# Kernel tuning notes

Measured on AMD Instinct MI355X. Metric: run time of the kernel, lower is better.

Reference implementation:

```python
import jax, jax.numpy as jnp
import numpy as np

B = 4; E_PER = 100_000; E = B * E_PER
N_NODES = 50_000; N_REL = 500; D = 64; D_LG = 256
K_PER_VI = 20; S_VI = E // K_PER_VI          # 20000 sorted vi segments
S_VJ_PER = 5_000; S_VJ = B * S_VJ_PER        # 20000 unsorted vj segments
N_MEM = 131_072
INTERACT = ((0, 3), (0, 2, 3), (0, 4), (0, 2, 4), (1, 3), (1, 2, 3), (1, 4), (1, 2, 4))


def _build_edges():
    rng = np.random.default_rng(0)
    idx_vi = np.repeat(np.arange(S_VI), K_PER_VI)          # sorted segment ids
    gpb = S_VI // B
    eg = idx_vi // gpb                                     # sorted by eg_idx too
    vi = rng.integers(0, N_NODES, S_VI)[idx_vi]
    idx_vj = np.empty(E, dtype=np.int64)
    for b in range(B):
        loc = np.concatenate([np.arange(S_VJ_PER), rng.integers(0, S_VJ_PER, E_PER - S_VJ_PER)])
        rng.shuffle(loc)
        idx_vj[b * E_PER:(b + 1) * E_PER] = b * S_VJ_PER + loc  # every group non-empty
    vj = rng.integers(0, N_NODES, S_VJ)[idx_vj]            # consistent (eg, vj) per group
    rel = rng.integers(0, N_REL, E)
    e2vi = rng.integers(0, N_MEM, E)
    e2vj = rng.integers(0, N_MEM, E)
    return np.stack([eg, vi, vj, rel, idx_vi, idx_vj, e2vi, e2vj], axis=1).astype(np.int32)


def setup_inputs() -> dict:
    key = jax.random.key(0)
    ks = jax.random.split(key, 10)
    return {
        "node_attention": jax.random.uniform(ks[0], (B, N_NODES), jnp.float32),
        "scanned_edges": jnp.asarray(_build_edges()),
        "edges_y": jax.random.uniform(ks[1], (E,), jnp.float32),
        "hidden_uncon": jax.random.normal(ks[2], (1, N_NODES, D_LG), jnp.float32),
        "hidden_con": jax.random.normal(ks[3], (N_MEM, D), jnp.float32),
        "Wc": jax.random.normal(ks[4], (D, D), jnp.float32) / np.sqrt(D).astype(np.float32),
        "bc": jnp.zeros((D,), jnp.float32),
        "Wu": jax.random.normal(ks[5], (D_LG, D), jnp.float32) / np.sqrt(D_LG).astype(np.float32),
        "bu": jnp.zeros((D,), jnp.float32),
        "rel_table": jax.random.normal(ks[6], (N_REL, D), jnp.float32) * 0.05,
        "ws": jax.random.normal(ks[7], (len(INTERACT), D), jnp.float32) / np.sqrt(float(len(INTERACT))).astype(np.float32) if False else jax.random.normal(ks[7], (len(INTERACT), D), jnp.float32) * (1.0 / np.sqrt(len(INTERACT)).astype(np.float32)),
        "fb": jnp.zeros((D,), jnp.float32),
        "out_w": jax.random.normal(ks[8], (D,), jnp.float32),
        "out_b": jnp.zeros((D,), jnp.float32),
        "n_vi_segments": S_VI,
        "n_vj_segments": S_VJ,
    }


def reference(node_attention, scanned_edges, edges_y, hidden_uncon, hidden_con,
              Wc, bc, Wu, bu, rel_table, ws, fb, out_w, out_b,
              n_vi_segments, n_vj_segments):
    eg, vi, vj, rel = (scanned_edges[:, i] for i in range(4))
    idx_vi, idx_vj, e2vi, e2vj = (scanned_edges[:, i] for i in range(4, 8))
    # projections (proj_con / proj_uncon, tanh Dense)
    hc = jnp.tanh(hidden_con @ Wc + bc)          # [N_MEM, D]
    hu = jnp.tanh(hidden_uncon @ Wu + bu)[0]     # [n_nodes, D]; batch_size==1 path of Node2Edge
    # Node2Edge gathers
    feats = (hc[e2vi], hu[vi], rel_table[rel], hc[e2vj], hu[vj])  # each [E, D]
    # F layer: weighted sum of elementwise interaction products
    out = fb
    for k, idxs in enumerate(INTERACT):
        x = feats[idxs[0]]
        for i in idxs[1:]:
            x = x * feats[i]
        out = out + x * ws[k]
    out = jax.nn.relu(out) * out_w + out_b
    logits = jnp.sum(out, axis=1)                # [E]
    # NeighborSoftmax at 'vi' (sorted segment softmax)
    m = jax.ops.segment_max(logits, idx_vi, num_segments=n_vi_segments)
    ex = jnp.exp(logits - m[idx_vi])
    den = jax.ops.segment_sum(ex, idx_vi, num_segments=n_vi_segments)
    transition = ex / den[idx_vi]
    # attention flow: gather source attention, weight, aggregate at vj
    trans_att = transition * node_attention[eg, vi] * edges_y
    aggr = jax.ops.segment_sum(trans_att, idx_vj, num_segments=n_vj_segments)
    b_g = jax.ops.segment_max(eg, idx_vj, num_segments=n_vj_segments)
    vj_g = jax.ops.segment_max(vj, idx_vj, num_segments=n_vj_segments)
    new_node_attention = jnp.zeros_like(node_attention).at[b_g, vj_g].add(aggr)
    return new_node_attention
```

## Files before the change

kernel.cpp:

```cpp
#include <hip/hip_runtime.h>
#include <hip/hip_bf16.h>
#include <type_traits>

#define D 64
#define KPER 20

typedef __attribute__((ext_vector_type(8))) short short8;
typedef __attribute__((ext_vector_type(4))) float floatx4;

__device__ __forceinline__ unsigned short f2bfu(float x) {
    __hip_bfloat16 h = __float2bfloat16(x);
    return *reinterpret_cast<unsigned short*>(&h);
}
__device__ __forceinline__ float bfu2f(unsigned short u) {
    return __uint_as_float(((unsigned)u) << 16);
}

__device__ __forceinline__ float fast_tanh(float x) {
    float xc = fminf(fmaxf(x, -15.f), 15.f);
    float e = __expf(2.f * xc);
    return 1.f - 2.f * __builtin_amdgcn_rcpf(1.f + e);
}

template<int CTRL>
__device__ __forceinline__ float dpp_add(float x) {
    int t = __builtin_amdgcn_update_dpp(0, __float_as_int(x), CTRL, 0xf, 0xf, true);
    return x + __int_as_float(t);
}
template<int CTRL>
__device__ __forceinline__ float dpp_max(float x) {
    int xi = __float_as_int(x);
    int t = __builtin_amdgcn_update_dpp(xi, xi, CTRL, 0xf, 0xf, false);
    return fmaxf(x, __int_as_float(t));
}
__device__ __forceinline__ float wave_sum_b(float x) {
    x = dpp_add<0x111>(x); x = dpp_add<0x112>(x);
    x = dpp_add<0x114>(x); x = dpp_add<0x118>(x);
    x = dpp_add<0x142>(x); x = dpp_add<0x143>(x);
    return __int_as_float(__builtin_amdgcn_readlane(__float_as_int(x), 63));
}
__device__ __forceinline__ float wave_max_b(float x) {
    x = dpp_max<0x111>(x); x = dpp_max<0x112>(x);
    x = dpp_max<0x114>(x); x = dpp_max<0x118>(x);
    x = dpp_max<0x142>(x); x = dpp_max<0x143>(x);
    return __int_as_float(__builtin_amdgcn_readlane(__float_as_int(x), 63));
}
__device__ __forceinline__ float row16_sum(float x) {
    x = dpp_add<0x111>(x); x = dpp_add<0x112>(x);
    x = dpp_add<0x114>(x); x = dpp_add<0x118>(x);
    return x;
}

__device__ __forceinline__ void proj64_pair(const float* __restrict__ h,
        const float* __restrict__ W, const float* __restrict__ b,
        unsigned short* __restrict__ out, int rt0) {
    constexpr int K = 64, KT = 2, CTN = 4;
    int lane = threadIdx.x & 63;
    int m = lane & 15, quad = lane >> 4;
    short8 bfr[CTN][KT];
    #pragma unroll
    for (int ct = 0; ct < CTN; ++ct)
        #pragma unroll
        for (int kt = 0; kt < KT; ++kt)
            #pragma unroll
            for (int j = 0; j < 8; ++j)
                bfr[ct][kt][j] = (short)f2bfu(W[(size_t)(kt * 32 + quad * 8 + j) * 64 + ct * 16 + m]);
    float bv[CTN];
    #pragma unroll
    for (int ct = 0; ct < CTN; ++ct) bv[ct] = b[ct * 16 + m];
    int rt1 = rt0 + 1;
    const float* hrow0 = h + (size_t)(rt0 * 16 + m) * K + quad * 8;
    const float* hrow1 = h + (size_t)(rt1 * 16 + m) * K + quad * 8;
    floatx4 a0[KT][2], a1[KT][2];
    #pragma unroll
    for (int kt = 0; kt < KT; ++kt) {
        a0[kt][0] = *(const floatx4*)(hrow0 + kt * 32);
        a0[kt][1] = *(const floatx4*)(hrow0 + kt * 32 + 4);
        a1[kt][0] = *(const floatx4*)(hrow1 + kt * 32);
        a1[kt][1] = *(const floatx4*)(hrow1 + kt * 32 + 4);
    }
    #pragma unroll
    for (int t = 0; t < 2; ++t) {
        floatx4 (*ar)[2] = t ? a1 : a0;
        int rt = t ? rt1 : rt0;
        floatx4 acc[CTN];
        #pragma unroll
        for (int ct = 0; ct < CTN; ++ct) acc[ct] = floatx4{0.f, 0.f, 0.f, 0.f};
        #pragma unroll
        for (int kt = 0; kt < KT; ++kt) {
            short8 af;
            #pragma unroll
            for (int j = 0; j < 4; ++j) {
                af[j]     = (short)f2bfu(ar[kt][0][j]);
                af[j + 4] = (short)f2bfu(ar[kt][1][j]);
            }
            #pragma unroll
            for (int ct = 0; ct < CTN; ++ct)
                acc[ct] = __builtin_amdgcn_mfma_f32_16x16x32_bf16(af, bfr[ct][kt], acc[ct], 0, 0, 0);
        }
        #pragma unroll
        for (int ct = 0; ct < CTN; ++ct) {
            int col = ct * 16 + m;
            #pragma unroll
            for (int reg = 0; reg < 4; ++reg) {
                int row = rt * 16 + quad * 4 + reg;
                out[(size_t)row * 64 + col] = f2bfu(fast_tanh(acc[ct][reg] + bv[ct]));
            }
        }
    }
}

__device__ __forceinline__ void proj256_body(const float* __restrict__ h,
        const float* __restrict__ W, const float* __restrict__ b,
        unsigned short* __restrict__ out, int ct0, int rt0, int rtstride, int ntiles) {
    constexpr int K = 256, KT = 8, CTN = 2;
    int lane = threadIdx.x & 63;
    int m = lane & 15, quad = lane >> 4;
    short8 bfr[CTN][KT];
    #pragma unroll
    for (int ct = 0; ct < CTN; ++ct)
        #pragma unroll
        for (int kt = 0; kt < KT; ++kt)
            #pragma unroll
            for (int j = 0; j < 8; ++j)
                bfr[ct][kt][j] = (short)f2bfu(W[(size_t)(kt * 32 + quad * 8 + j) * 64 + (ct0 + ct) * 16 + m]);
    float bv[CTN];
    #pragma unroll
    for (int ct = 0; ct < CTN; ++ct) bv[ct] = b[(ct0 + ct) * 16 + m];
    for (int rt = rt0; rt < ntiles; rt += rtstride) {
        floatx4 acc[CTN];
        #pragma unroll
        for (int ct = 0; ct < CTN; ++ct) acc[ct] = floatx4{0.f, 0.f, 0.f, 0.f};
        const float* hrow = h + (size_t)(rt * 16 + m) * K + quad * 8;
        #pragma unroll
        for (int kt = 0; kt < KT; ++kt) {
            floatx4 v0 = *(const floatx4*)(hrow + kt * 32);
            floatx4 v1 = *(const floatx4*)(hrow + kt * 32 + 4);
            short8 af;
            #pragma unroll
            for (int j = 0; j < 4; ++j) {
                af[j]     = (short)f2bfu(v0[j]);
                af[j + 4] = (short)f2bfu(v1[j]);
            }
            #pragma unroll
            for (int ct = 0; ct < CTN; ++ct)
                acc[ct] = __builtin_amdgcn_mfma_f32_16x16x32_bf16(af, bfr[ct][kt], acc[ct], 0, 0, 0);
        }
        #pragma unroll
        for (int ct = 0; ct < CTN; ++ct) {
            int col = (ct0 + ct) * 16 + m;
            #pragma unroll
            for (int reg = 0; reg < 4; ++reg) {
                int row = rt * 16 + quad * 4 + reg;
                out[(size_t)row * 64 + col] = f2bfu(fast_tanh(acc[ct][reg] + bv[ct]));
            }
        }
    }
}

#define RELB 16
#define ZB 8
__global__ __launch_bounds__(256) void proj_fused(
        const float* __restrict__ hcon, const float* __restrict__ Wc, const float* __restrict__ bc,
        const float* __restrict__ hun, const float* __restrict__ Wu, const float* __restrict__ bu,
        const float* __restrict__ relf, unsigned short* __restrict__ hc,
        unsigned short* __restrict__ hu, unsigned short* __restrict__ relb,
        float* __restrict__ outz, int nout,
        int t64, int t256, int g64, int g256, int nrel) {
    int bid = blockIdx.x;
    int w = threadIdx.x >> 6;
    if (bid < g64) {
        int wid = bid * 4 + w;
        proj64_pair(hcon, Wc, bc, hc, wid * 2);
    } else if (bid < g64 + g256) {
        int wid = (bid - g64) * 4 + w;
        int half = wid & 1;
        proj256_body(hun, Wu, bu, hu, half * 2, wid >> 1, (g256 * 4) >> 1, t256);
    } else if (bid < g64 + g256 + RELB) {
        int tid = (bid - g64 - g256) * 256 + threadIdx.x;
        for (int i = tid; i < nrel; i += RELB * 256) relb[i] = f2bfu(relf[i]);
    } else {
        int tid = (bid - g64 - g256 - RELB) * 256 + threadIdx.x;
        for (int i = tid; i < nout; i += ZB * 256) outz[i] = 0.0f;
    }
}

__device__ __forceinline__ void unp4(uint2 u, float f[4]) {
    f[0] = __uint_as_float(u.x << 16);
    f[1] = __uint_as_float(u.x & 0xffff0000u);
    f[2] = __uint_as_float(u.y << 16);
    f[3] = __uint_as_float(u.y & 0xffff0000u);
}

__global__ __launch_bounds__(256) void edge_kernel(
        const float* __restrict__ natt, const int* __restrict__ edges,
        const float* __restrict__ ey, const unsigned short* __restrict__ hc,
        const unsigned short* __restrict__ hu, const unsigned short* __restrict__ relt,
        const float* __restrict__ wsm, const float* __restrict__ fb,
        const float* __restrict__ outw, float* __restrict__ out, int N) {
    int lane = threadIdx.x & 63;
    int g = lane >> 4, sub = lane & 15;
    int l2 = lane >> 2;
    int s = blockIdx.x * 4 + (threadIdx.x >> 6);
    long base = (long)s * KPER;
    const int* eb = edges + base * 8;
    int eg = __builtin_amdgcn_readfirstlane(eb[0]);
    int vi = __builtin_amdgcn_readfirstlane(eb[1]);

    const int* ebg = eb + g * 8;
    int vjx[5], relx[5], evix[5], evjx[5];
    #pragma unroll
    for (int i = 0; i < 5; ++i) {
        vjx[i]  = ebg[i * 32 + 2];
        relx[i] = ebg[i * 32 + 3];
        evix[i] = ebg[i * 32 + 6];
        evjx[i] = ebg[i * 32 + 7];
    }
    uint2 G0[5], G2[5], G3[5], G4[5];
    #pragma unroll
    for (int i = 0; i < 5; ++i) {
        G0[i] = *(const uint2*)(hc   + (size_t)evix[i] * D + sub * 4);
        G2[i] = *(const uint2*)(relt + (size_t)relx[i] * D + sub * 4);
        G3[i] = *(const uint2*)(hc   + (size_t)evjx[i] * D + sub * 4);
        G4[i] = *(const uint2*)(hu   + (size_t)vjx[i]  * D + sub * 4);
    }
    uint2 F1u = *(const uint2*)(hu + (size_t)vi * D + sub * 4);
    float f1[4];
    unp4(F1u, f1);

    floatx4 wv[8];
    #pragma unroll
    for (int k = 0; k < 8; ++k) wv[k] = *(const floatx4*)(wsm + k * D + sub * 4);
    floatx4 fbv = *(const floatx4*)(fb + sub * 4);
    floatx4 owv = *(const floatx4*)(outw + sub * 4);
    float na = natt[(size_t)eg * N + vi];

    float myl = -INFINITY;
    #pragma unroll
    for (int i = 0; i < 5; ++i) {
        float F0[4], F2[4], F3[4], F4[4];
        unp4(G0[i], F0); unp4(G2[i], F2); unp4(G3[i], F3); unp4(G4[i], F4);
        float acc = 0.f;
        #pragma unroll
        for (int j = 0; j < 4; ++j) {
            float t1 = fmaf(F2[j], wv[1][j], wv[0][j]);
            float t2 = fmaf(F2[j], wv[5][j], wv[4][j]);
            float t3 = fmaf(F2[j], wv[3][j], wv[2][j]);
            float t4 = fmaf(F2[j], wv[7][j], wv[6][j]);
            float u = fmaf(F0[j], t1, f1[j] * t2);
            float v = fmaf(F0[j], t3, f1[j] * t4);
            float od = fmaf(F3[j], u, fmaf(F4[j], v, fbv[j]));
            acc = fmaf(fmaxf(od, 0.f), owv[j], acc);
        }
        float rs = row16_sum(acc);
        float tot = __shfl(rs, ((lane & 3) << 4) + 15);
        myl = (l2 == i) ? tot : myl;
    }
    float mx = wave_max_b(myl);
    float ex = __expf(myl - mx);
    float den = wave_sum_b(ex);
    if (lane < KPER) {
        int myvj = eb[lane * 8 + 2];
        float t = (ex / den) * na * ey[base + lane];
        atomicAdd(out + (size_t)eg * N + myvj, t);
    }
}

extern "C" void kernel_launch(void* const* d_in, const int* in_sizes, int n_in,
                              void* d_out, int out_size, void* d_ws, size_t ws_size,
                              hipStream_t stream) {
    const float* natt = (const float*)d_in[0];
    const int*   edges = (const int*)d_in[1];
    const float* ey   = (const float*)d_in[2];
    const float* hun  = (const float*)d_in[3];
    const float* hcon = (const float*)d_in[4];
    const float* Wc   = (const float*)d_in[5];
    const float* bc   = (const float*)d_in[6];
    const float* Wu   = (const float*)d_in[7];
    const float* bu   = (const float*)d_in[8];
    const float* relt = (const float*)d_in[9];
    const float* wsm  = (const float*)d_in[10];
    const float* fb   = (const float*)d_in[11];
    const float* outw = (const float*)d_in[12];
    float* out = (float*)d_out;

    int E    = in_sizes[2];
    int S    = E / KPER;
    int nmem = in_sizes[4] / D;
    int N    = in_sizes[3] / 256;
    int nrel = in_sizes[9];

    int t64  = nmem / 16;
    int t256 = N / 16;
    int g64  = t64 / 8;
    int g256 = 512;

    unsigned short* hc = (unsigned short*)d_ws;
    unsigned short* hu = hc + (size_t)nmem * D;
    unsigned short* rb = hu + (size_t)N * D;

    proj_fused<<<g64 + g256 + RELB + ZB, 256, 0, stream>>>(hcon, Wc, bc, hun, Wu, bu,
                                                           relt, hc, hu, rb,
                                                           out, out_size,
                                                           t64, t256, g64, g256, nrel);
    edge_kernel<<<S / 4, 256, 0, stream>>>(natt, edges, ey, hc, hu, rb,
                                           wsm, fb, outw, out, N);
}
```

Measured before the change: 203.6 us.

## Pre-pack bf16 MFMA weight fragments in a prep kernel and reorder projection blocks

Adds a small prep kernel that converts Wc and Wu to bf16 once, in MFMA fragment order, and also handles the relation-table conversion and output zeroing. The projection waves then load each B fragment with one vector load instead of eight strided scalar loads plus conversions. The 256-wide projection blocks are placed first and their count rises from 512 to 800. This adds one extra kernel launch and a dependency between launches in exchange for cheaper per-wave weight setup.

```diff
diff --git a/kernel.cpp b/kernel.cpp
--- a/kernel.cpp
+++ b/kernel.cpp
@@ -51,8 +51,32 @@
     return x;
 }
 
+__global__ __launch_bounds__(256) void prep(
+        const float* __restrict__ Wc, const float* __restrict__ Wu,
+        const float* __restrict__ relf,
+        unsigned short* __restrict__ Wcp, unsigned short* __restrict__ Wup,
+        unsigned short* __restrict__ relb, float* __restrict__ outz,
+        int nout, int nrel) {
+    int tid = blockIdx.x * 256 + threadIdx.x;
+    int nth = gridDim.x * 256;
+    for (int i = tid; i < 4 * 2 * 64 * 8; i += nth) {
+        int j = i & 7, lane = (i >> 3) & 63, f = i >> 9;
+        int ct = f >> 1, kt = f & 1;
+        int m = lane & 15, quad = lane >> 4;
+        Wcp[i] = f2bfu(Wc[(kt * 32 + quad * 8 + j) * 64 + ct * 16 + m]);
+    }
+    for (int i = tid; i < 4 * 8 * 64 * 8; i += nth) {
+        int j = i & 7, lane = (i >> 3) & 63, f = i >> 9;
+        int ct = f >> 3, kt = f & 7;
+        int m = lane & 15, quad = lane >> 4;
+        Wup[i] = f2bfu(Wu[(kt * 32 + quad * 8 + j) * 64 + ct * 16 + m]);
+    }
+    for (int i = tid; i < nrel; i += nth) relb[i] = f2bfu(relf[i]);
+    for (int i = tid; i < nout; i += nth) outz[i] = 0.0f;
+}
+
 __device__ __forceinline__ void proj64_pair(const float* __restrict__ h,
-        const float* __restrict__ W, const float* __restrict__ b,
+        const unsigned short* __restrict__ Wp, const float* __restrict__ b,
         unsigned short* __restrict__ out, int rt0) {
     constexpr int K = 64, KT = 2, CTN = 4;
     int lane = threadIdx.x & 63;
@@ -62,9 +86,7 @@
     for (int ct = 0; ct < CTN; ++ct)
         #pragma unroll
         for (int kt = 0; kt < KT; ++kt)
-            #pragma unroll
-            for (int j = 0; j < 8; ++j)
-                bfr[ct][kt][j] = (short)f2bfu(W[(size_t)(kt * 32 + quad * 8 + j) * 64 + ct * 16 + m]);
+            bfr[ct][kt] = *(const short8*)(Wp + (((ct * 2 + kt) * 64 + lane) << 3));
     float bv[CTN];
     #pragma unroll
     for (int ct = 0; ct < CTN; ++ct) bv[ct] = b[ct * 16 + m];
@@ -111,7 +133,7 @@
 }
 
 __device__ __forceinline__ void proj256_body(const float* __restrict__ h,
-        const float* __restrict__ W, const float* __restrict__ b,
+        const unsigned short* __restrict__ Wp, const float* __restrict__ b,
         unsigned short* __restrict__ out, int ct0, int rt0, int rtstride, int ntiles) {
     constexpr int K = 256, KT = 8, CTN = 2;
     int lane = threadIdx.x & 63;
@@ -121,9 +143,7 @@
     for (int ct = 0; ct < CTN; ++ct)
         #pragma unroll
         for (int kt = 0; kt < KT; ++kt)
-            #pragma unroll
-            for (int j = 0; j < 8; ++j)
-                bfr[ct][kt][j] = (short)f2bfu(W[(size_t)(kt * 32 + quad * 8 + j) * 64 + (ct0 + ct) * 16 + m]);
+            bfr[ct][kt] = *(const short8*)(Wp + ((((ct0 + ct) * 8 + kt) * 64 + lane) << 3));
     float bv[CTN];
     #pragma unroll
     for (int ct = 0; ct < CTN; ++ct) bv[ct] = b[(ct0 + ct) * 16 + m];
@@ -158,30 +178,22 @@
     }
 }
 
-#define RELB 16
-#define ZB 8
 __global__ __launch_bounds__(256) void proj_fused(
-        const float* __restrict__ hcon, const float* __restrict__ Wc, const float* __restrict__ bc,
-        const float* __restrict__ hun, const float* __restrict__ Wu, const float* __restrict__ bu,
-        const float* __restrict__ relf, unsigned short* __restrict__ hc,
-        unsigned short* __restrict__ hu, unsigned short* __restrict__ relb,
-        float* __restrict__ outz, int nout,
-        int t64, int t256, int g64, int g256, int nrel) {
+        const float* __restrict__ hcon, const unsigned short* __restrict__ Wcp,
+        const float* __restrict__ bc,
+        const float* __restrict__ hun, const unsigned short* __restrict__ Wup,
+        const float* __restrict__ bu,
+        unsigned short* __restrict__ hc, unsigned short* __restrict__ hu,
+        int t64, int t256, int g64, int g256) {
     int bid = blockIdx.x;
     int w = threadIdx.x >> 6;
-    if (bid < g64) {
+    if (bid < g256) {
         int wid = bid * 4 + w;
-        proj64_pair(hcon, Wc, bc, hc, wid * 2);
-    } else if (bid < g64 + g256) {
-        int wid = (bid - g64) * 4 + w;
         int half = wid & 1;
-        proj256_body(hun, Wu, bu, hu, half * 2, wid >> 1, (g256 * 4) >> 1, t256);
-    } else if (bid < g64 + g256 + RELB) {
-        int tid = (bid - g64 - g256) * 256 + threadIdx.x;
-        for (int i = tid; i < nrel; i += RELB * 256) relb[i] = f2bfu(relf[i]);
+        proj256_body(hun, Wup, bu, hu, half * 2, wid >> 1, g256 * 2, t256);
     } else {
-        int tid = (bid - g64 - g256 - RELB) * 256 + threadIdx.x;
-        for (int i = tid; i < nout; i += ZB * 256) outz[i] = 0.0f;
+        int wid = (bid - g256) * 4 + w;
+        proj64_pair(hcon, Wcp, bc, hc, wid * 2);
     }
 }
 
@@ -293,16 +305,17 @@
     int t64  = nmem / 16;
     int t256 = N / 16;
     int g64  = t64 / 8;
-    int g256 = 512;
-
-    unsigned short* hc = (unsigned short*)d_ws;
-    unsigned short* hu = hc + (size_t)nmem * D;
-    unsigned short* rb = hu + (size_t)N * D;
-
-    proj_fused<<<g64 + g256 + RELB + ZB, 256, 0, stream>>>(hcon, Wc, bc, hun, Wu, bu,
-                                                           relt, hc, hu, rb,
-                                                           out, out_size,
-                                                           t64, t256, g64, g256, nrel);
+    int g256 = 800;
+
+    unsigned short* hc  = (unsigned short*)d_ws;
+    unsigned short* hu  = hc + (size_t)nmem * D;
+    unsigned short* rb  = hu + (size_t)N * D;
+    unsigned short* Wcp = rb + nrel;
+    unsigned short* Wup = Wcp + 4096;
+
+    prep<<<64, 256, 0, stream>>>(Wc, Wu, relt, Wcp, Wup, rb, out, out_size, nrel);
+    proj_fused<<<g256 + g64, 256, 0, stream>>>(hcon, Wcp, bc, hun, Wup, bu,
+                                               hc, hu, t64, t256, g64, g256);
     edge_kernel<<<S / 4, 256, 0, stream>>>(natt, edges, ey, hc, hu, rb,
                                            wsm, fb, outw, out, N);
 }
```

After: 201.4 us. No clear change (-1.0%).
